# Kernel tuning notes

Measured on AMD Instinct MI355X. Metric: run time of the kernel, lower is better.

Reference implementation:

```python
import jax, jax.numpy as jnp
import numpy as np

# Architecture constants (from init_kwargs)
B, L, D = 4, 2048, 512          # docs, tokens per doc, embed_dim
H = 8                           # num_heads -> head_dim 64
HALF_WIN = (33 - 1) // 2        # window_size=33 -> 16 keys each side
GAP = 1 + 1                     # dilation_gap=1 -> step 2
OVERLAP = HALF_WIN * GAP        # 32
W = 2 * HALF_WIN                # 32 keys per token (self excluded)


def setup_inputs() -> dict:
    key = jax.random.key(0)
    ks = jax.random.split(key, 5)
    s = 0.02
    return {
        "begin": jax.random.normal(ks[0], (B, OVERLAP, D), dtype=jnp.float32),
        "main": jax.random.normal(ks[1], (B, L, D), dtype=jnp.float32),
        "end": jax.random.normal(ks[2], (B, OVERLAP, D), dtype=jnp.float32),
        "in_proj_w": jax.random.normal(ks[3], (3 * D, D), dtype=jnp.float32) * s,
        "in_proj_b": jnp.zeros((3 * D,), dtype=jnp.float32),
        "out_proj_w": jax.random.normal(ks[4], (D, D), dtype=jnp.float32) * s,
        "out_proj_b": jnp.zeros((D,), dtype=jnp.float32),
    }


def reference(begin, main, end, in_proj_w, in_proj_b, out_proj_w, out_proj_b):
    hd = D // H
    # padded[b, overlap + t] == main[b, t]; begin/end provide halo context.
    padded = jnp.concatenate([begin, main, end], axis=1)  # [B, L+2*OVERLAP, D]

    # Static dilated-window gather indices (matches the shifted-cat loops).
    offsets = np.concatenate(
        [np.arange(-OVERLAP, 0, GAP), np.arange(GAP, OVERLAP + GAP, GAP)]
    )  # [W]
    idx = np.arange(L)[:, None] + offsets[None, :] + OVERLAP  # [L, W]

    wq, wk, wv = jnp.split(in_proj_w, 3, axis=0)   # each [D, D]
    bq, bk, bv = jnp.split(in_proj_b, 3, axis=0)

    q = main @ wq.T + bq                            # [B, L, D]
    k_full = padded @ wk.T + bk                     # project once, then gather
    v_full = padded @ wv.T + bv
    k = k_full[:, idx]                              # [B, L, W, D]
    v = v_full[:, idx]                              # [B, L, W, D]

    qh = q.reshape(B, L, H, hd)
    kh = k.reshape(B, L, W, H, hd)
    vh = v.reshape(B, L, W, H, hd)

    scores = jnp.einsum('blhd,blwhd->blhw', qh, kh) / jnp.sqrt(jnp.float32(hd))
    attn = jax.nn.softmax(scores, axis=-1)          # [B, L, H, W]
    o = jnp.einsum('blhw,blwhd->blhd', attn, vh).reshape(B, L, D)
    o = o @ out_proj_w.T + out_proj_b               # [B, L, D]

    # cat(main, attn_out) per token, then concat docs along dim 0.
    return jnp.concatenate([main, o], axis=-1).reshape(B * L, 2 * D)
```

## Files before the change

### kernel.cpp

```cpp
#include <hip/hip_runtime.h>

typedef unsigned short u16;
typedef unsigned int u32;
typedef __attribute__((ext_vector_type(8))) __bf16 bf16x8;
typedef __attribute__((ext_vector_type(4))) float f32x4;

#define NB 4
#define SEQ 2048
#define DIM 512
#define NH 8
#define HD 64
#define OV 32
#define PD 2112

#define PACK_N (NB * PD * (DIM / 4))
#define WIN_N (3 * DIM * DIM / 4)
#define WOUT_N (DIM * DIM / 4)

#define GLL(g, l)                                                  \
  __builtin_amdgcn_global_load_lds(                                \
      (const __attribute__((address_space(1))) void*)(g),          \
      (__attribute__((address_space(3))) void*)(l), 16, 0, 0)

__device__ __forceinline__ u16 f2bf(float f) {
  union { float f; u32 u; } x; x.f = f;
  u32 r = x.u + 0x7fffu + ((x.u >> 16) & 1u);
  return (u16)(r >> 16);
}

__global__ void k_prep(const float* __restrict__ begin,
                       const float* __restrict__ mainp,
                       const float* __restrict__ endp,
                       const float* __restrict__ w_in_f,
                       const float* __restrict__ w_out_f,
                       u16* __restrict__ pad,
                       u16* __restrict__ w_in,
                       u16* __restrict__ w_out) {
  int i = blockIdx.x * 256 + threadIdx.x;
  const float* src;
  u16* dst;
  if (i < PACK_N) {
    int d4 = (i & 127) * 4;
    int p = (i >> 7) % PD;
    int b = i / (PD * (DIM / 4));
    if (p < OV)            src = begin + ((size_t)(b * OV + p)) * DIM + d4;
    else if (p < OV + SEQ) src = mainp + ((size_t)(b * SEQ + (p - OV))) * DIM + d4;
    else                   src = endp + ((size_t)(b * OV + (p - OV - SEQ))) * DIM + d4;
    dst = pad + (size_t)i * 4;
  } else if (i < PACK_N + WIN_N) {
    int j = i - PACK_N;
    src = w_in_f + (size_t)j * 4;
    dst = w_in + (size_t)j * 4;
  } else if (i < PACK_N + WIN_N + WOUT_N) {
    int j = i - PACK_N - WIN_N;
    src = w_out_f + (size_t)j * 4;
    dst = w_out + (size_t)j * 4;
  } else {
    return;
  }
  float4 v = *(const float4*)src;
  u32 lo = (u32)f2bf(v.x) | ((u32)f2bf(v.y) << 16);
  u32 hi = (u32)f2bf(v.z) | ((u32)f2bf(v.w) << 16);
  *(uint2*)dst = make_uint2(lo, hi);
}


__device__ __forceinline__ void gemm_loop_sb(const u16* __restrict__ A,
                                             const u16* __restrict__ Bw,
                                             int tm0, int tn0,
                                             u16* __restrict__ As, u16* __restrict__ Bs,
                                             f32x4 acc[4][4]) {
  const int tid = threadIdx.x;
  const int lane = tid & 63;
  const int w = tid >> 6;
  const int rr = lane & 15, g = lane >> 4;
  const int wm = (w >> 1) * 64, wn = (w & 1) * 64;
  const int srow = tid >> 3;
  const int lg = (tid & 7) ^ (srow & 7);
  const u16* gA = A + (size_t)(tm0 + srow) * 512 + lg * 8;
  const u16* gB = Bw + (size_t)(tn0 + srow) * 512 + lg * 8;
  char* lA = (char*)As + w * 1024;
  char* lB = (char*)Bs + w * 1024;
#pragma unroll 1
  for (int t = 0; t < 8; ++t) {
#pragma unroll
    for (int j = 0; j < 4; ++j) {
      GLL(gA + (size_t)j * 32 * 512 + t * 64, lA + j * 4096);
      GLL(gB + (size_t)j * 32 * 512 + t * 64, lB + j * 4096);
    }
    __syncthreads();
    bf16x8 af[4][2], bfr[4][2];
#pragma unroll
    for (int f = 0; f < 4; ++f) {
#pragma unroll
      for (int ks = 0; ks < 2; ++ks) {
        int ra = wm + f * 16 + rr;
        int rb = wn + f * 16 + rr;
        af[f][ks] = *(const bf16x8*)&As[ra * 64 + (((ks * 4 + g) ^ (ra & 7)) << 3)];
        bfr[f][ks] = *(const bf16x8*)&Bs[rb * 64 + (((ks * 4 + g) ^ (rb & 7)) << 3)];
      }
    }
#pragma unroll
    for (int ks = 0; ks < 2; ++ks)
#pragma unroll
      for (int fm = 0; fm < 4; ++fm)
#pragma unroll
        for (int fn = 0; fn < 4; ++fn)
          acc[fm][fn] = __builtin_amdgcn_mfma_f32_16x16x32_bf16(af[fm][ks], bfr[fn][ks], acc[fm][fn], 0, 0, 0);
    __syncthreads();
  }
}

__global__ __launch_bounds__(256) void k_gemm_qkv(const u16* __restrict__ A,
                                                  const u16* __restrict__ Bw,
                                                  const float* __restrict__ bias,
                                                  u16* __restrict__ qh,
                                                  u16* __restrict__ kh,
                                                  u16* __restrict__ vt) {
  __shared__ __align__(16) u16 smem[17408];
  const int bx = blockIdx.x;
  const int tm0 = (bx / 12) * 128, tn0 = (bx % 12) * 128;
  f32x4 acc[4][4] = {};
  gemm_loop_sb(A, Bw, tm0, tn0, smem, smem + 8192, acc);

  const int tid = threadIdx.x, lane = tid & 63, wv = tid >> 6;
  const int rr = lane & 15, g = lane >> 4;
  const int wm = (wv >> 1) * 64, wn = (wv & 1) * 64;
#pragma unroll
  for (int fm = 0; fm < 4; ++fm)
#pragma unroll
    for (int fn = 0; fn < 4; ++fn) {
      float bb = bias[tn0 + wn + fn * 16 + rr];
#pragma unroll
      for (int r = 0; r < 4; ++r)
        smem[(wm + fm * 16 + g * 4 + r) * 136 + wn + fn * 16 + rr] = f2bf(acc[fm][fn][r] + bb);
    }
  __syncthreads();

  const int reg = tn0 >> 9;
  if (reg < 2) {
    int r2 = tid >> 1, hf = tid & 1;
    int grow = tm0 + r2;
    int b = grow / PD, p = grow - b * PD;
    int cb = (tn0 & 511) + hf * 64;
    int h = cb >> 6;
    const uint4* s = (const uint4*)&smem[r2 * 136 + hf * 64];
    u16* dst = nullptr;
    if (reg == 1) dst = kh + (((size_t)(b * NH + h)) * PD + p) * HD;
    else if (p >= OV && p < OV + SEQ) dst = qh + (((size_t)(b * NH + h)) * SEQ + (p - OV)) * HD;
    if (dst) {
#pragma unroll
      for (int i = 0; i < 8; ++i) ((uint4*)dst)[i] = s[i];
    }
  } else {
    int col = tid >> 1;
    int rb = (tid & 1) * 64;
    int c = (tn0 & 511) + col;
    int h = c >> 6, d = c & 63;
#pragma unroll
    for (int ch = 0; ch < 8; ++ch) {
      int grow = tm0 + rb + ch * 8;
      int b = grow / PD, p0 = grow - b * PD;
      u32 w4[4];
#pragma unroll
      for (int i = 0; i < 4; ++i) {
        u32 lo = smem[(rb + ch * 8 + 2 * i) * 136 + col];
        u32 hi = smem[(rb + ch * 8 + 2 * i + 1) * 136 + col];
        w4[i] = lo | (hi << 16);
      }
      *(uint4*)&vt[(((size_t)(b * NH + h)) * HD + d) * PD + p0] = *(uint4*)w4;
    }
  }
}

__global__ __launch_bounds__(256) void k_gemm_oproj(const u16* __restrict__ A,
                                                    const u16* __restrict__ Bw,
                                                    const float* __restrict__ bias,
                                                    const float* __restrict__ mainp,
                                                    float* __restrict__ out) {
  __shared__ __align__(16) u16 smem[16384];
  int bx = blockIdx.x;
  int tm0 = (bx >> 2) * 128, tn0 = (bx & 3) * 128;
  for (int i = threadIdx.x; i < 4096; i += 256) {
    int r = i >> 5, c4 = (i & 31) * 4;
    *(float4*)&out[(size_t)(tm0 + r) * 1024 + tn0 + c4] =
        *(const float4*)&mainp[(size_t)(tm0 + r) * 512 + tn0 + c4];
  }
  f32x4 acc[4][4] = {};
  gemm_loop_sb(A, Bw, tm0, tn0, smem, smem + 8192, acc);
  int lane = threadIdx.x & 63, wv = threadIdx.x >> 6;
  int rr = lane & 15, g = lane >> 4;
  int wm = (wv >> 1) * 64, wn = (wv & 1) * 64;
#pragma unroll
  for (int fm = 0; fm < 4; ++fm)
#pragma unroll
    for (int fn = 0; fn < 4; ++fn) {
      int j = tn0 + wn + fn * 16 + rr;
      float bb = bias[j];
#pragma unroll
      for (int r = 0; r < 4; ++r) {
        int row = tm0 + wm + fm * 16 + g * 4 + r;
        out[(size_t)row * 1024 + 512 + j] = acc[fm][fn][r] + bb;
      }
    }
}

__device__ __forceinline__ int pswz(int slot, int key) {
  return (slot < 8) ? (slot ^ (key & 7)) : ((slot & 12) | ((slot ^ (key & 3)) & 3));
}

__global__ __launch_bounds__(256) void k_attn(const u16* __restrict__ qh,
                                              const u16* __restrict__ kh,
                                              const u16* __restrict__ vt,
                                              u16* __restrict__ ob) {
  __shared__ __align__(16) u16 Ks[128 * 64];
  __shared__ __align__(16) u16 Vs[64 * 128];
  __shared__ __align__(16) u16 Qs[64 * 64];
  __shared__ __align__(16) u16 Ps[4 * 16 * 96];
  const int tid = threadIdx.x;
  const int lane = tid & 63;
  const int wq = tid >> 6;
  const int g = lane >> 4, qi = lane & 15;
  const int bx = blockIdx.x;
  const int tile = bx & 31, h = (bx >> 5) & 7, b = bx >> 8;
  const int l0 = tile * 64;
  const size_t bh = (size_t)(b * NH + h);

  {
    const u16* kg = kh + (bh * PD + l0) * HD;
#pragma unroll
    for (int i = 0; i < 4; ++i) {
      int c = tid + 256 * i;
      int row = c >> 3, slot = c & 7;
      *(uint4*)&Ks[row * 64 + ((slot ^ (row & 7)) << 3)] =
          *(const uint4*)&kg[(size_t)row * HD + slot * 8];
    }
    const u16* vg = vt + bh * HD * PD + l0;
#pragma unroll
    for (int i = 0; i < 4; ++i) {
      int c = tid + 256 * i;
      int d = c >> 4, slot = c & 15;
      *(uint4*)&Vs[d * 128 + ((slot ^ (d & 15)) << 3)] =
          *(const uint4*)&vg[(size_t)d * PD + slot * 8];
    }
    const u16* qg = qh + (bh * SEQ + l0) * HD;
#pragma unroll
    for (int i = 0; i < 2; ++i) {
      int c = tid + 256 * i;
      int row = c >> 3, slot = c & 7;
      *(uint4*)&Qs[row * 64 + ((slot ^ (row & 7)) << 3)] =
          *(const uint4*)&qg[(size_t)row * HD + slot * 8];
    }
  }
  __syncthreads();

  bf16x8 bq[2];
  {
    int qrow = 16 * wq + qi;
#pragma unroll
    for (int ks = 0; ks < 2; ++ks)
      bq[ks] = *(const bf16x8*)&Qs[qrow * 64 + ((((g + 4 * ks)) ^ (qrow & 7)) << 3)];
  }
  f32x4 sa[5];
#pragma unroll
  for (int tt = 0; tt < 5; ++tt) { f32x4 z = {0.f, 0.f, 0.f, 0.f}; sa[tt] = z; }
#pragma unroll
  for (int tt = 0; tt < 5; ++tt) {
    int krow = 16 * (wq + tt) + qi;
#pragma unroll
    for (int ks = 0; ks < 2; ++ks) {
      bf16x8 ak = *(const bf16x8*)&Ks[krow * 64 + (((g + 4 * ks) ^ (krow & 7)) << 3)];
      sa[tt] = __builtin_amdgcn_mfma_f32_16x16x32_bf16(ak, bq[ks], sa[tt], 0, 0, 0);
    }
  }

  float m = -1e30f;
#pragma unroll
  for (int tt = 0; tt < 5; ++tt)
#pragma unroll
    for (int r = 0; r < 4; ++r) {
      int rel = 16 * tt + 4 * g + r - qi;
      bool val = (rel >= 0) && (rel <= 64) && (rel != 32) && ((rel & 1) == 0);
      if (val) m = fmaxf(m, sa[tt][r]);
    }
  m = fmaxf(m, __shfl_xor(m, 16));
  m = fmaxf(m, __shfl_xor(m, 32));
  float p[5][4];
  float sum = 0.f;
#pragma unroll
  for (int tt = 0; tt < 5; ++tt)
#pragma unroll
    for (int r = 0; r < 4; ++r) {
      int rel = 16 * tt + 4 * g + r - qi;
      bool val = (rel >= 0) && (rel <= 64) && (rel != 32) && ((rel & 1) == 0);
      p[tt][r] = val ? __expf((sa[tt][r] - m) * 0.125f) : 0.f;
      sum += p[tt][r];
    }
  sum += __shfl_xor(sum, 16);
  sum += __shfl_xor(sum, 32);
  float inv = 1.f / sum;

  {
    int prow = 16 * wq + qi;
    int colb = (wq & 1) << 4;
#pragma unroll
    for (int tt = 0; tt < 5; ++tt) {
#pragma unroll
      for (int pp = 0; pp < 2; ++pp) {
        int e = 4 * g + 2 * pp;
        int slot = ((colb + 16 * tt) >> 3) + (e >> 3);
        int swz = pswz(slot, qi);
        u32 w = (u32)f2bf(p[tt][2 * pp] * inv) | ((u32)f2bf(p[tt][2 * pp + 1] * inv) << 16);
        *(u32*)&Ps[prow * 96 + swz * 8 + (e & 7)] = w;
      }
    }
    int zslot = ((wq & 1) ? 0 : 10) + ((lane >> 4) & 1);
    int half = lane >> 5;
    int swz = pswz(zslot, qi);
    uint2 z2 = make_uint2(0u, 0u);
    *(uint2*)&Ps[(16 * wq + qi) * 96 + swz * 8 + half * 4] = z2;
  }
  __syncthreads();

  f32x4 oa[4];
#pragma unroll
  for (int dt = 0; dt < 4; ++dt) { f32x4 z = {0.f, 0.f, 0.f, 0.f}; oa[dt] = z; }
  int kbo = (wq >= 2) ? 1 : 0;
#pragma unroll
  for (int kt = 0; kt < 3; ++kt) {
    int slot = 4 * kt + g;
    int swz = pswz(slot, qi);
    bf16x8 pa = *(const bf16x8*)&Ps[(16 * wq + qi) * 96 + swz * 8];
    int sabs = 4 * (kt + kbo) + g;
#pragma unroll
    for (int dt = 0; dt < 4; ++dt) {
      int d = 16 * dt + qi;
      bf16x8 bv = *(const bf16x8*)&Vs[d * 128 + ((sabs ^ (d & 15)) << 3)];
      oa[dt] = __builtin_amdgcn_mfma_f32_16x16x32_bf16(pa, bv, oa[dt], 0, 0, 0);
    }
  }

  u16* og = ob + ((size_t)b * SEQ + l0 + 16 * wq) * DIM + h * HD;
#pragma unroll
  for (int dt = 0; dt < 4; ++dt)
#pragma unroll
    for (int r = 0; r < 4; ++r) {
      int qo = 4 * g + r;
      og[(size_t)qo * DIM + 16 * dt + qi] = f2bf(oa[dt][r]);
    }
}

extern "C" void kernel_launch(void* const* d_in, const int* in_sizes, int n_in,
                              void* d_out, int out_size, void* d_ws, size_t ws_size,
                              hipStream_t stream) {
  const float* begin = (const float*)d_in[0];
  const float* mainp = (const float*)d_in[1];
  const float* endp = (const float*)d_in[2];
  const float* w_in_f = (const float*)d_in[3];
  const float* b_in = (const float*)d_in[4];
  const float* w_out_f = (const float*)d_in[5];
  const float* b_out = (const float*)d_in[6];
  float* out = (float*)d_out;

  char* ws = (char*)d_ws;
  u16* pad_bf = (u16*)ws; ws += (size_t)NB * PD * DIM * 2;
  u16* w_in = (u16*)ws;   ws += (size_t)3 * DIM * DIM * 2;
  u16* w_out = (u16*)ws;  ws += (size_t)DIM * DIM * 2;
  u16* qhb = (u16*)ws;    ws += (size_t)NB * NH * SEQ * HD * 2;
  u16* khb = (u16*)ws;    ws += (size_t)NB * NH * PD * HD * 2;
  u16* vtb = (u16*)ws;    ws += (size_t)NB * NH * HD * PD * 2;
  u16* ob = (u16*)ws;     ws += (size_t)NB * SEQ * DIM * 2;

  k_prep<<<(PACK_N + WIN_N + WOUT_N + 255) / 256, 256, 0, stream>>>(
      begin, mainp, endp, w_in_f, w_out_f, pad_bf, w_in, w_out);
  k_gemm_qkv<<<66 * 12, 256, 0, stream>>>(pad_bf, w_in, b_in, qhb, khb, vtb);
  k_attn<<<NB * NH * (SEQ / 64), 256, 0, stream>>>(qhb, khb, vtb, ob);
  k_gemm_oproj<<<64 * 4, 256, 0, stream>>>(ob, w_out, b_out, mainp, out);
}
```

Baseline: 71.93 us.

## Store QKV projection row-major and transpose V in attention LDS load

```diff
diff --git a/kernel.cpp b/kernel.cpp
--- a/kernel.cpp
+++ b/kernel.cpp
@@ -64,7 +64,6 @@
   *(uint2*)dst = make_uint2(lo, hi);
 }
 
-
 __device__ __forceinline__ void gemm_loop_sb(const u16* __restrict__ A,
                                              const u16* __restrict__ Bw,
                                              int tm0, int tn0,
@@ -114,9 +113,7 @@
 __global__ __launch_bounds__(256) void k_gemm_qkv(const u16* __restrict__ A,
                                                   const u16* __restrict__ Bw,
                                                   const float* __restrict__ bias,
-                                                  u16* __restrict__ qh,
-                                                  u16* __restrict__ kh,
-                                                  u16* __restrict__ vt) {
+                                                  u16* __restrict__ Cb) {
   __shared__ __align__(16) u16 smem[17408];
   const int bx = blockIdx.x;
   const int tm0 = (bx / 12) * 128, tn0 = (bx % 12) * 128;
@@ -136,40 +133,12 @@
         smem[(wm + fm * 16 + g * 4 + r) * 136 + wn + fn * 16 + rr] = f2bf(acc[fm][fn][r] + bb);
     }
   __syncthreads();
-
-  const int reg = tn0 >> 9;
-  if (reg < 2) {
+  {
     int r2 = tid >> 1, hf = tid & 1;
-    int grow = tm0 + r2;
-    int b = grow / PD, p = grow - b * PD;
-    int cb = (tn0 & 511) + hf * 64;
-    int h = cb >> 6;
+    u16* dst = Cb + (size_t)(tm0 + r2) * 1536 + tn0 + hf * 64;
     const uint4* s = (const uint4*)&smem[r2 * 136 + hf * 64];
-    u16* dst = nullptr;
-    if (reg == 1) dst = kh + (((size_t)(b * NH + h)) * PD + p) * HD;
-    else if (p >= OV && p < OV + SEQ) dst = qh + (((size_t)(b * NH + h)) * SEQ + (p - OV)) * HD;
-    if (dst) {
-#pragma unroll
-      for (int i = 0; i < 8; ++i) ((uint4*)dst)[i] = s[i];
-    }
-  } else {
-    int col = tid >> 1;
-    int rb = (tid & 1) * 64;
-    int c = (tn0 & 511) + col;
-    int h = c >> 6, d = c & 63;
-#pragma unroll
-    for (int ch = 0; ch < 8; ++ch) {
-      int grow = tm0 + rb + ch * 8;
-      int b = grow / PD, p0 = grow - b * PD;
-      u32 w4[4];
-#pragma unroll
-      for (int i = 0; i < 4; ++i) {
-        u32 lo = smem[(rb + ch * 8 + 2 * i) * 136 + col];
-        u32 hi = smem[(rb + ch * 8 + 2 * i + 1) * 136 + col];
-        w4[i] = lo | (hi << 16);
-      }
-      *(uint4*)&vt[(((size_t)(b * NH + h)) * HD + d) * PD + p0] = *(uint4*)w4;
-    }
+#pragma unroll
+    for (int i = 0; i < 8; ++i) ((uint4*)dst)[i] = s[i];
   }
 }
 
@@ -209,9 +178,7 @@
   return (slot < 8) ? (slot ^ (key & 7)) : ((slot & 12) | ((slot ^ (key & 3)) & 3));
 }
 
-__global__ __launch_bounds__(256) void k_attn(const u16* __restrict__ qh,
-                                              const u16* __restrict__ kh,
-                                              const u16* __restrict__ vt,
+__global__ __launch_bounds__(256) void k_attn(const u16* __restrict__ Cb,
                                               u16* __restrict__ ob) {
   __shared__ __align__(16) u16 Ks[128 * 64];
   __shared__ __align__(16) u16 Vs[64 * 128];
@@ -224,32 +191,37 @@
   const int bx = blockIdx.x;
   const int tile = bx & 31, h = (bx >> 5) & 7, b = bx >> 8;
   const int l0 = tile * 64;
-  const size_t bh = (size_t)(b * NH + h);
 
   {
-    const u16* kg = kh + (bh * PD + l0) * HD;
+    const u16* kb = Cb + ((size_t)b * PD + l0) * 1536 + 512 + h * 64;
 #pragma unroll
     for (int i = 0; i < 4; ++i) {
       int c = tid + 256 * i;
       int row = c >> 3, slot = c & 7;
       *(uint4*)&Ks[row * 64 + ((slot ^ (row & 7)) << 3)] =
-          *(const uint4*)&kg[(size_t)row * HD + slot * 8];
-    }
-    const u16* vg = vt + bh * HD * PD + l0;
+          *(const uint4*)&kb[(size_t)row * 1536 + slot * 8];
+    }
+    const u16* vb = Cb + ((size_t)b * PD + l0) * 1536 + 1024 + h * 64;
 #pragma unroll
     for (int i = 0; i < 4; ++i) {
       int c = tid + 256 * i;
-      int d = c >> 4, slot = c & 15;
-      *(uint4*)&Vs[d * 128 + ((slot ^ (d & 15)) << 3)] =
-          *(const uint4*)&vg[(size_t)d * PD + slot * 8];
-    }
-    const u16* qg = qh + (bh * SEQ + l0) * HD;
+      int row = c >> 3, dg = c & 7;
+      uint4 v = *(const uint4*)&vb[(size_t)row * 1536 + dg * 8];
+      u32 wds[4] = {v.x, v.y, v.z, v.w};
+#pragma unroll
+      for (int j = 0; j < 8; ++j) {
+        int d = dg * 8 + j;
+        u16 val = (u16)(wds[j >> 1] >> ((j & 1) * 16));
+        Vs[d * 128 + (((row >> 3) ^ (d & 15)) << 3) + (row & 7)] = val;
+      }
+    }
+    const u16* qb = Cb + ((size_t)b * PD + OV + l0) * 1536 + h * 64;
 #pragma unroll
     for (int i = 0; i < 2; ++i) {
       int c = tid + 256 * i;
       int row = c >> 3, slot = c & 7;
       *(uint4*)&Qs[row * 64 + ((slot ^ (row & 7)) << 3)] =
-          *(const uint4*)&qg[(size_t)row * HD + slot * 8];
+          *(const uint4*)&qb[(size_t)row * 1536 + slot * 8];
     }
   }
   __syncthreads();
@@ -366,14 +338,12 @@
   u16* pad_bf = (u16*)ws; ws += (size_t)NB * PD * DIM * 2;
   u16* w_in = (u16*)ws;   ws += (size_t)3 * DIM * DIM * 2;
   u16* w_out = (u16*)ws;  ws += (size_t)DIM * DIM * 2;
-  u16* qhb = (u16*)ws;    ws += (size_t)NB * NH * SEQ * HD * 2;
-  u16* khb = (u16*)ws;    ws += (size_t)NB * NH * PD * HD * 2;
-  u16* vtb = (u16*)ws;    ws += (size_t)NB * NH * HD * PD * 2;
+  u16* Cb = (u16*)ws;     ws += (size_t)NB * PD * 3 * DIM * 2;
   u16* ob = (u16*)ws;     ws += (size_t)NB * SEQ * DIM * 2;
 
   k_prep<<<(PACK_N + WIN_N + WOUT_N + 255) / 256, 256, 0, stream>>>(
       begin, mainp, endp, w_in_f, w_out_f, pad_bf, w_in, w_out);
-  k_gemm_qkv<<<66 * 12, 256, 0, stream>>>(pad_bf, w_in, b_in, qhb, khb, vtb);
-  k_attn<<<NB * NH * (SEQ / 64), 256, 0, stream>>>(qhb, khb, vtb, ob);
+  k_gemm_qkv<<<66 * 12, 256, 0, stream>>>(pad_bf, w_in, b_in, Cb);
+  k_attn<<<NB * NH * (SEQ / 64), 256, 0, stream>>>(Cb, ob);
   k_gemm_oproj<<<64 * 4, 256, 0, stream>>>(ob, w_out, b_out, mainp, out);
 }
```

Result: slower. 74.07 us (+3.0%).
